# Optimization experiments

Measured on AMD Instinct MI355X. Metric: run time of the kernel, lower is better.

Reference implementation:

```python
import jax, jax.numpy as jnp
import numpy as np

N_NODES = 100000
N_EDGES = 1600000
D = 64
K = 10


def setup_inputs() -> dict:
    key = jax.random.key(0)
    k1, k2, k3, k4 = jax.random.split(key, 4)
    features = jax.random.normal(k1, (N_NODES, D), dtype=jnp.float32)
    s = jax.random.normal(k2, (D, 1), dtype=jnp.float32)
    src = jax.random.randint(k3, (N_EDGES,), 0, N_NODES, dtype=jnp.int64)
    dst = jax.random.randint(k4, (N_EDGES,), 0, N_NODES, dtype=jnp.int64)
    return {"features": features, "s": s, "src": src, "dst": dst, "k": K}


def reference(features, s, src, dst, k):
    n = features.shape[0]
    # symmetric degree norm: deg_in clamped at 1, norm = deg^{-1/2}
    deg = jax.ops.segment_sum(jnp.ones_like(dst, dtype=features.dtype), dst,
                              num_segments=n)
    norm = jnp.power(jnp.maximum(deg, 1.0), -0.5)[:, None]  # [N,1]

    def step(h, _):
        h = h * norm
        # copy_u + sum: scatter-add src features into dst nodes (SpMM)
        h = jax.ops.segment_sum(h[src], dst, num_segments=n)
        h = h * norm
        return h, h

    _, hops = jax.lax.scan(step, features, None, length=k)  # [k,N,D]
    H = jnp.concatenate([features[None], hops], axis=0)      # [k+1,N,D]
    H = jnp.transpose(H, (1, 0, 2))                           # [N,k+1,D]
    # attention pooling: S = sigmoid(H @ s), out = S^T H
    S = jax.nn.sigmoid(jnp.einsum('nkd,d->nk', H, s[:, 0]))  # [N,k+1]
    out = jnp.einsum('nk,nkd->nd', S, H)                      # [N,D]
    return out
```

## Files before the change

### kernel.cpp

```cpp
#include <hip/hip_runtime.h>
#include <hip/hip_fp16.h>
#include <math.h>

#define D 64
#define RB 1024
#define EB 2048
#define NRMAX 128
#define KHOPS 10


typedef union { uint4 u; __half2 h[4]; } U4H;
typedef float vfloat2 __attribute__((ext_vector_type(2)));

__device__ __forceinline__ void acc_fp8x8(uint2 q, float* a) {
    vfloat2 r0 = __builtin_amdgcn_cvt_pk_f32_fp8(q.x, false);
    vfloat2 r1 = __builtin_amdgcn_cvt_pk_f32_fp8(q.x, true);
    vfloat2 r2 = __builtin_amdgcn_cvt_pk_f32_fp8(q.y, false);
    vfloat2 r3 = __builtin_amdgcn_cvt_pk_f32_fp8(q.y, true);
    a[0] += r0.x; a[1] += r0.y; a[2] += r1.x; a[3] += r1.y;
    a[4] += r2.x; a[5] += r2.y; a[6] += r3.x; a[7] += r3.y;
}

__device__ __forceinline__ uint2 pack_fp8x8(const float* v) {
    uint2 q;
    q.x = __builtin_amdgcn_cvt_pk_fp8_f32(v[0], v[1], 0, false);
    q.x = __builtin_amdgcn_cvt_pk_fp8_f32(v[2], v[3], q.x, true);
    q.y = __builtin_amdgcn_cvt_pk_fp8_f32(v[4], v[5], 0, false);
    q.y = __builtin_amdgcn_cvt_pk_fp8_f32(v[6], v[7], q.y, true);
    return q;
}


__global__ void countA(const int* __restrict__ dst, int* __restrict__ countsA_T,
                       int E, int NR, int NBLK) {
    __shared__ int hist[NRMAX];
    int t = threadIdx.x;
    for (int i = t; i < NR; i += 256) hist[i] = 0;
    __syncthreads();
    int base = blockIdx.x * EB + t;
    #pragma unroll
    for (int j = 0; j < EB / 256; ++j) {
        int e = base + j * 256;
        if (e < E) atomicAdd(&hist[dst[e] >> 10], 1);
    }
    __syncthreads();
    for (int i = t; i < NR; i += 256) countsA_T[i * NBLK + blockIdx.x] = hist[i];
}

__global__ void block_sums(const int* __restrict__ arr, int* __restrict__ bsum, int n) {
    int base = blockIdx.x * 1024;
    int t = threadIdx.x;
    int v = 0;
    #pragma unroll
    for (int j = 0; j < 4; ++j) {
        int i = base + t + j * 256;
        if (i < n) v += arr[i];
    }
    #pragma unroll
    for (int m = 32; m >= 1; m >>= 1) v += __shfl_xor(v, m, 64);
    __shared__ int ws[4];
    if ((t & 63) == 0) ws[t >> 6] = v;
    __syncthreads();
    if (t == 0) bsum[blockIdx.x] = ws[0] + ws[1] + ws[2] + ws[3];
}

__global__ void scan_bsums(int* __restrict__ bsum, int nb) {
    __shared__ int tmp[1024];
    int t = threadIdx.x;
    int v = (t < nb) ? bsum[t] : 0;
    tmp[t] = v;
    __syncthreads();
    for (int off = 1; off < 1024; off <<= 1) {
        int x = (t >= off) ? tmp[t - off] : 0;
        __syncthreads();
        tmp[t] += x;
        __syncthreads();
    }
    if (t < nb) bsum[t] = tmp[t] - v;
}

__global__ void gen_scan2(const int* __restrict__ arr, const int* __restrict__ bsum,
                          int* __restrict__ out, int n) {
    __shared__ int tmp[1024];
    int base = blockIdx.x * 1024;
    int t = threadIdx.x;
    int i = base + t;
    int v = (i < n) ? arr[i] : 0;
    tmp[t] = v;
    __syncthreads();
    for (int off = 1; off < 1024; off <<= 1) {
        int x = (t >= off) ? tmp[t - off] : 0;
        __syncthreads();
        tmp[t] += x;
        __syncthreads();
    }
    if (i < n) out[i] = bsum[blockIdx.x] + tmp[t] - v;
}

__global__ void passA2(const int* __restrict__ src, const int* __restrict__ dst,
                       const int* __restrict__ baseA, unsigned int* __restrict__ ebuf2,
                       int E, int NR, int NBLK) {
    __shared__ int cur[NRMAX];
    int t = threadIdx.x;
    for (int i = t; i < NR; i += 256) cur[i] = baseA[i * NBLK + blockIdx.x];
    __syncthreads();
    int base = blockIdx.x * EB + t;
    #pragma unroll
    for (int j = 0; j < EB / 256; ++j) {
        int e = base + j * 256;
        if (e < E) {
            int v = dst[e];
            int pos = atomicAdd(&cur[v >> 10], 1);
            ebuf2[pos] = (unsigned int)src[e] | ((unsigned int)(v & (RB - 1)) << 17);
        }
    }
}

__global__ void range_build(const unsigned int* __restrict__ ebuf2,
                            const int* __restrict__ baseA,
                            int* __restrict__ offsets, float* __restrict__ norm,
                            int* __restrict__ csr, int N, int E, int NR, int NBLK) {
    __shared__ int cnt[RB];
    __shared__ int sc[RB];
    int rg = blockIdx.x;
    int t = threadIdx.x;
    int r0 = baseA[rg * NBLK];
    int r1 = (rg + 1 < NR) ? baseA[(rg + 1) * NBLK] : E;
    cnt[t] = 0;
    __syncthreads();
    for (int i = r0 + t; i < r1; i += RB)
        atomicAdd(&cnt[ebuf2[i] >> 17], 1);
    __syncthreads();
    int v = cnt[t];
    sc[t] = v;
    __syncthreads();
    for (int off = 1; off < RB; off <<= 1) {
        int x = (t >= off) ? sc[t - off] : 0;
        __syncthreads();
        sc[t] += x;
        __syncthreads();
    }
    int excl = sc[t] - v;
    int node = rg * RB + t;
    if (node < N) {
        offsets[node] = r0 + excl;
        norm[node] = rsqrtf((float)(v > 1 ? v : 1));
    }
    if (rg == NR - 1 && t == 0) offsets[N] = E;
    __syncthreads();
    cnt[t] = r0 + excl;
    __syncthreads();
    for (int i = r0 + t; i < r1; i += RB) {
        unsigned int u = ebuf2[i];
        int pos = atomicAdd(&cnt[u >> 17], 1);
        csr[pos] = (int)(u & 0x1FFFFu);
    }
}


__global__ void hop0(const float4* __restrict__ feat, const float* __restrict__ s,
                     const float* __restrict__ norm, uint4* __restrict__ g0,
                     uint2* __restrict__ p0, float4* __restrict__ out,
                     int n, int do_pool, int write8) {
    int t = blockIdx.x * blockDim.x + threadIdx.x;
    int node = t >> 3;
    int l = t & 7;
    if (node >= n) return;
    float4 f0 = feat[node * 16 + 2 * l];
    float4 f1 = feat[node * 16 + 2 * l + 1];
    float nv = norm[node];
    float v[8] = {f0.x * nv, f0.y * nv, f0.z * nv, f0.w * nv,
                  f1.x * nv, f1.y * nv, f1.z * nv, f1.w * nv};
    U4H P;
    P.h[0] = __floats2half2_rn(v[0], v[1]);
    P.h[1] = __floats2half2_rn(v[2], v[3]);
    P.h[2] = __floats2half2_rn(v[4], v[5]);
    P.h[3] = __floats2half2_rn(v[6], v[7]);
    g0[node * 8 + l] = P.u;
    if (write8) p0[node * 8 + l] = pack_fp8x8(v);
    if (do_pool) {
        const float4* s4 = (const float4*)s;
        float4 a = s4[2 * l], b = s4[2 * l + 1];
        float dot = f0.x * a.x + f0.y * a.y + f0.z * a.z + f0.w * a.w
                  + f1.x * b.x + f1.y * b.y + f1.z * b.z + f1.w * b.w;
        #pragma unroll
        for (int m = 1; m <= 4; m <<= 1) dot += __shfl_xor(dot, m, 64);
        float sig = 1.0f / (1.0f + expf(-dot));
        out[node * 16 + 2 * l]     = make_float4(sig * f0.x, sig * f0.y, sig * f0.z, sig * f0.w);
        out[node * 16 + 2 * l + 1] = make_float4(sig * f1.x, sig * f1.y, sig * f1.z, sig * f1.w);
    }
}


#define FP8_SLOT(K)                                                        \
    {                                                                      \
        int e0 = g + 8 * (K), e1 = e0 + 8;                                 \
        int u0 = __shfl(idx, e0, 64);                                      \
        int u1 = __shfl(idx, e1, 64);                                      \
        uint2 q0 = gin8[(size_t)u0 * 8 + l];                               \
        uint2 q1 = gin8[(size_t)u1 * 8 + l];                               \
        if (e0 < dcap) acc_fp8x8(q0, acc);                                 \
        if (e1 < dcap) acc_fp8x8(q1, acc);                                 \
    }

__global__ void spmm_hop_fp8(const uint2* __restrict__ gin8,
                             const int* __restrict__ offsets,
                             const int* __restrict__ csr,
                             const float* __restrict__ norm,
                             uint4* __restrict__ gout16,
                             uint2* __restrict__ gout8,
                             int n, int write8) {
    int lane = threadIdx.x & 63;
    int node = blockIdx.x * 4 + (threadIdx.x >> 6);
    if (node >= n) return;
    int g = lane >> 3;
    int l = lane & 7;
    int beg = offsets[node], end = offsets[node + 1];
    int deg = end - beg;
    int dcap = deg < 64 ? deg : 64;
    int idx = (lane < dcap) ? csr[beg + lane] : 0;

    float acc[8] = {0.f, 0.f, 0.f, 0.f, 0.f, 0.f, 0.f, 0.f};
    FP8_SLOT(0)
    if (dcap > 16) FP8_SLOT(2)
    if (dcap > 32) { FP8_SLOT(4) FP8_SLOT(6) }
    for (int i = beg + 64 + g; i < end; i += 8) {
        acc_fp8x8(gin8[(size_t)csr[i] * 8 + l], acc);
    }

    #pragma unroll
    for (int m = 8; m <= 32; m <<= 1) {
        #pragma unroll
        for (int jj = 0; jj < 8; ++jj) acc[jj] += __shfl_xor(acc[jj], m, 64);
    }

    if (g == 0) {
        float nv = norm[node];
        float gv[8];
        #pragma unroll
        for (int jj = 0; jj < 8; ++jj) gv[jj] = acc[jj] * nv * nv;
        U4H P;
        P.h[0] = __floats2half2_rn(gv[0], gv[1]);
        P.h[1] = __floats2half2_rn(gv[2], gv[3]);
        P.h[2] = __floats2half2_rn(gv[4], gv[5]);
        P.h[3] = __floats2half2_rn(gv[6], gv[7]);
        gout16[node * 8 + l] = P.u;
        if (write8) gout8[node * 8 + l] = pack_fp8x8(gv);
    }
}


__global__ void spmm_hop(const uint4* __restrict__ gin, const int* __restrict__ offsets,
                         const int* __restrict__ csr, const float* __restrict__ norm,
                         const float* __restrict__ s, uint4* __restrict__ gout,
                         float4* __restrict__ out, int n, int do_pool, int write_g) {
    int lane = threadIdx.x & 63;
    int node = blockIdx.x * 4 + (threadIdx.x >> 6);
    if (node >= n) return;
    int g = lane >> 3;
    int l = lane & 7;
    int beg = offsets[node], end = offsets[node + 1];
    int deg = end - beg;
    int dcap = deg < 64 ? deg : 64;
    int idx = (lane < dcap) ? csr[beg + lane] : 0;

    __half2 z = __floats2half2_rn(0.f, 0.f);
    __half2 ah0 = z, ah1 = z, ah2 = z, ah3 = z;
    {
        int e0 = g, e1 = g + 8, e2 = g + 16, e3 = g + 24;
        int u0 = __shfl(idx, e0, 64);
        int u1 = __shfl(idx, e1, 64);
        int u2 = __shfl(idx, e2, 64);
        int u3 = __shfl(idx, e3, 64);
        U4H A, B, C, Dd;
        A.u = gin[(size_t)u0 * 8 + l];
        B.u = gin[(size_t)u1 * 8 + l];
        C.u = gin[(size_t)u2 * 8 + l];
        Dd.u = gin[(size_t)u3 * 8 + l];
        if (e0 < dcap) { ah0 = __hadd2(ah0, A.h[0]); ah1 = __hadd2(ah1, A.h[1]); ah2 = __hadd2(ah2, A.h[2]); ah3 = __hadd2(ah3, A.h[3]); }
        if (e1 < dcap) { ah0 = __hadd2(ah0, B.h[0]); ah1 = __hadd2(ah1, B.h[1]); ah2 = __hadd2(ah2, B.h[2]); ah3 = __hadd2(ah3, B.h[3]); }
        if (e2 < dcap) { ah0 = __hadd2(ah0, C.h[0]); ah1 = __hadd2(ah1, C.h[1]); ah2 = __hadd2(ah2, C.h[2]); ah3 = __hadd2(ah3, C.h[3]); }
        if (e3 < dcap) { ah0 = __hadd2(ah0, Dd.h[0]); ah1 = __hadd2(ah1, Dd.h[1]); ah2 = __hadd2(ah2, Dd.h[2]); ah3 = __hadd2(ah3, Dd.h[3]); }
    }
    if (dcap > 32) {
        int e0 = g + 32, e1 = g + 40, e2 = g + 48, e3 = g + 56;
        int u0 = __shfl(idx, e0, 64);
        int u1 = __shfl(idx, e1, 64);
        int u2 = __shfl(idx, e2, 64);
        int u3 = __shfl(idx, e3, 64);
        U4H A, B, C, Dd;
        A.u = gin[(size_t)u0 * 8 + l];
        B.u = gin[(size_t)u1 * 8 + l];
        C.u = gin[(size_t)u2 * 8 + l];
        Dd.u = gin[(size_t)u3 * 8 + l];
        if (e0 < dcap) { ah0 = __hadd2(ah0, A.h[0]); ah1 = __hadd2(ah1, A.h[1]); ah2 = __hadd2(ah2, A.h[2]); ah3 = __hadd2(ah3, A.h[3]); }
        if (e1 < dcap) { ah0 = __hadd2(ah0, B.h[0]); ah1 = __hadd2(ah1, B.h[1]); ah2 = __hadd2(ah2, B.h[2]); ah3 = __hadd2(ah3, B.h[3]); }
        if (e2 < dcap) { ah0 = __hadd2(ah0, C.h[0]); ah1 = __hadd2(ah1, C.h[1]); ah2 = __hadd2(ah2, C.h[2]); ah3 = __hadd2(ah3, C.h[3]); }
        if (e3 < dcap) { ah0 = __hadd2(ah0, Dd.h[0]); ah1 = __hadd2(ah1, Dd.h[1]); ah2 = __hadd2(ah2, Dd.h[2]); ah3 = __hadd2(ah3, Dd.h[3]); }
    }

    float2 q0 = __half22float2(ah0), q1 = __half22float2(ah1);
    float2 q2 = __half22float2(ah2), q3 = __half22float2(ah3);
    float acc[8] = {q0.x, q0.y, q1.x, q1.y, q2.x, q2.y, q3.x, q3.y};

    for (int i = beg + 64 + g; i < end; i += 8) {
        U4H P; P.u = gin[(size_t)csr[i] * 8 + l];
        float2 a0 = __half22float2(P.h[0]), a1 = __half22float2(P.h[1]);
        float2 a2 = __half22float2(P.h[2]), a3 = __half22float2(P.h[3]);
        acc[0] += a0.x; acc[1] += a0.y; acc[2] += a1.x; acc[3] += a1.y;
        acc[4] += a2.x; acc[5] += a2.y; acc[6] += a3.x; acc[7] += a3.y;
    }

    #pragma unroll
    for (int m = 8; m <= 32; m <<= 1) {
        #pragma unroll
        for (int jj = 0; jj < 8; ++jj) acc[jj] += __shfl_xor(acc[jj], m, 64);
    }

    float nv = norm[node];
    float h[8];
    #pragma unroll
    for (int jj = 0; jj < 8; ++jj) h[jj] = acc[jj] * nv;

    float sig = 0.f;
    if (do_pool) {
        const float4* s4 = (const float4*)s;
        float4 a = s4[2 * l], b = s4[2 * l + 1];
        float dot = h[0] * a.x + h[1] * a.y + h[2] * a.z + h[3] * a.w
                  + h[4] * b.x + h[5] * b.y + h[6] * b.z + h[7] * b.w;
        #pragma unroll
        for (int m = 1; m <= 4; m <<= 1) dot += __shfl_xor(dot, m, 64);
        sig = 1.0f / (1.0f + expf(-dot));
    }

    if (g == 0) {
        if (write_g) {
            U4H P;
            P.h[0] = __floats2half2_rn(h[0] * nv, h[1] * nv);
            P.h[1] = __floats2half2_rn(h[2] * nv, h[3] * nv);
            P.h[2] = __floats2half2_rn(h[4] * nv, h[5] * nv);
            P.h[3] = __floats2half2_rn(h[6] * nv, h[7] * nv);
            gout[node * 8 + l] = P.u;
        }
        if (do_pool) {
            float4 o0 = out[node * 16 + 2 * l];
            float4 o1 = out[node * 16 + 2 * l + 1];
            o0.x += sig * h[0]; o0.y += sig * h[1]; o0.z += sig * h[2]; o0.w += sig * h[3];
            o1.x += sig * h[4]; o1.y += sig * h[5]; o1.z += sig * h[6]; o1.w += sig * h[7];
            out[node * 16 + 2 * l]     = o0;
            out[node * 16 + 2 * l + 1] = o1;
        }
    }
}


__global__ void pool_epilogue(const uint4* __restrict__ gbase, size_t gstride,
                              const float* __restrict__ norm,
                              const float* __restrict__ s,
                              float4* __restrict__ out, int N) {
    int t0 = blockIdx.x * blockDim.x + threadIdx.x;
    int node = t0 >> 3;
    int l = t0 & 7;
    if (node >= N) return;
    float inv_nv = 1.0f / norm[node];
    const float4* s4 = (const float4*)s;
    float4 sa = s4[2 * l], sb = s4[2 * l + 1];
    float o[8] = {0.f, 0.f, 0.f, 0.f, 0.f, 0.f, 0.f, 0.f};
    for (int t = 0; t <= KHOPS; ++t) {
        U4H P; P.u = gbase[(size_t)t * gstride + (size_t)node * 8 + l];
        float2 a0 = __half22float2(P.h[0]), a1 = __half22float2(P.h[1]);
        float2 a2 = __half22float2(P.h[2]), a3 = __half22float2(P.h[3]);
        float gf[8] = {a0.x, a0.y, a1.x, a1.y, a2.x, a2.y, a3.x, a3.y};
        float dot = gf[0] * sa.x + gf[1] * sa.y + gf[2] * sa.z + gf[3] * sa.w
                  + gf[4] * sb.x + gf[5] * sb.y + gf[6] * sb.z + gf[7] * sb.w;
        #pragma unroll
        for (int m = 1; m <= 4; m <<= 1) dot += __shfl_xor(dot, m, 64);
        float sig = 1.0f / (1.0f + expf(-dot * inv_nv));
        float sc = sig * inv_nv;
        #pragma unroll
        for (int j = 0; j < 8; ++j) o[j] += sc * gf[j];
    }
    out[node * 16 + 2 * l]     = make_float4(o[0], o[1], o[2], o[3]);
    out[node * 16 + 2 * l + 1] = make_float4(o[4], o[5], o[6], o[7]);
}


extern "C" void kernel_launch(void* const* d_in, const int* in_sizes, int n_in,
                              void* d_out, int out_size, void* d_ws, size_t ws_size,
                              hipStream_t stream) {
    const float* feat = (const float*)d_in[0];
    const float* s    = (const float*)d_in[1];
    const int*   src  = (const int*)d_in[2];
    const int*   dst  = (const int*)d_in[3];

    int N = in_sizes[0] / D;
    int E = in_sizes[2];
    int NR   = (N + RB - 1) / RB;
    int NBLK = (E + EB - 1) / EB;
    int M    = NR * NBLK;
    int nchA = (M + 1023) / 1024;

    int*   offsets  = (int*)d_ws;
    int*   csr      = offsets + (N + 1);
    float* norm     = (float*)(csr + E);
    int*   countsA  = (int*)(norm + N);
    int*   baseA    = countsA + M;
    int*   bsumA    = baseA + M;
    uintptr_t p = (uintptr_t)(bsumA + nchA);
    p = (p + 255) & ~(uintptr_t)255;
    uint4* gbase = (uint4*)p;
    size_t gstride = (size_t)N * 8;
    uint2* pbase = (uint2*)(gbase + (size_t)(KHOPS + 1) * gstride);
    size_t pstride = (size_t)N * 8;

    size_t fixed_bytes = (uintptr_t)gbase - (uintptr_t)d_ws;
    size_t need_f16 = (size_t)(KHOPS + 1) * gstride * sizeof(uint4);
    size_t need_fp8 = 2 * pstride * sizeof(uint2);
    int mode;
    if (ws_size >= fixed_bytes + need_f16 + need_fp8) mode = 2;
    else if (ws_size >= fixed_bytes + need_f16)       mode = 1;
    else                                              mode = 0;

    unsigned int* ebuf2 = (unsigned int*)(gbase + gstride);

    countA<<<NBLK, 256, 0, stream>>>(dst, countsA, E, NR, NBLK);
    block_sums<<<nchA, 256, 0, stream>>>(countsA, bsumA, M);
    scan_bsums<<<1, 1024, 0, stream>>>(bsumA, nchA);
    gen_scan2<<<nchA, 1024, 0, stream>>>(countsA, bsumA, baseA, M);
    passA2<<<NBLK, 256, 0, stream>>>(src, dst, baseA, ebuf2, E, NR, NBLK);
    range_build<<<NR, RB, 0, stream>>>(ebuf2, baseA, offsets, norm, csr, N, E, NR, NBLK);

    float4* outp = (float4*)d_out;
    int nb_node8 = (N * 8 + 255) / 256;
    int nb_spmm  = (N + 3) / 4;

    if (mode == 2) {
        hop0<<<nb_node8, 256, 0, stream>>>((const float4*)feat, s, norm, gbase,
                                           pbase, outp, N, 0, 1);
        for (int t = 0; t < KHOPS; ++t) {
            spmm_hop_fp8<<<nb_spmm, 256, 0, stream>>>(
                pbase + (size_t)(t & 1) * pstride, offsets, csr, norm,
                gbase + (size_t)(t + 1) * gstride,
                pbase + (size_t)((t + 1) & 1) * pstride,
                N, (t < KHOPS - 1) ? 1 : 0);
        }
        pool_epilogue<<<nb_node8, 256, 0, stream>>>(gbase, gstride, norm, s, outp, N);
    } else if (mode == 1) {
        hop0<<<nb_node8, 256, 0, stream>>>((const float4*)feat, s, norm, gbase,
                                           (uint2*)nullptr, outp, N, 0, 0);
        for (int t = 0; t < KHOPS; ++t) {
            spmm_hop<<<nb_spmm, 256, 0, stream>>>(
                gbase + (size_t)t * gstride, offsets, csr, norm, s,
                gbase + (size_t)(t + 1) * gstride, outp, N, 0, 1);
        }
        pool_epilogue<<<nb_node8, 256, 0, stream>>>(gbase, gstride, norm, s, outp, N);
    } else {
        hop0<<<nb_node8, 256, 0, stream>>>((const float4*)feat, s, norm, gbase,
                                           (uint2*)nullptr, outp, N, 1, 0);
        uint4* gin = gbase;
        uint4* gout = gbase + gstride;
        for (int t = 0; t < KHOPS; ++t) {
            spmm_hop<<<nb_spmm, 256, 0, stream>>>(
                gin, offsets, csr, norm, s, gout, outp, N, 1, (t < KHOPS - 1) ? 1 : 0);
            uint4* tmp = gin; gin = gout; gout = tmp;
        }
    }
}
```

Measured before the change: 546.0 us.

## Make fp8 SpMM hop persistent with grid-stride nodes and prefetched next indices

```diff
diff --git a/kernel.cpp b/kernel.cpp
--- a/kernel.cpp
+++ b/kernel.cpp
@@ -7,6 +7,7 @@
 #define EB 2048
 #define NRMAX 128
 #define KHOPS 10
+#define HOP_BLOCKS 2048
 
 
 typedef union { uint4 u; __half2 h[4]; } U4H;
@@ -192,164 +193,96 @@
 }
 
 
-#define FP8_SLOT(K)                                                        \
-    {                                                                      \
-        int e0 = g + 8 * (K), e1 = e0 + 8;                                 \
-        int u0 = __shfl(idx, e0, 64);                                      \
-        int u1 = __shfl(idx, e1, 64);                                      \
-        uint2 q0 = gin8[(size_t)u0 * 8 + l];                               \
-        uint2 q1 = gin8[(size_t)u1 * 8 + l];                               \
-        if (e0 < dcap) acc_fp8x8(q0, acc);                                 \
-        if (e1 < dcap) acc_fp8x8(q1, acc);                                 \
-    }
-
 __global__ void spmm_hop_fp8(const uint2* __restrict__ gin8,
                              const int* __restrict__ offsets,
                              const int* __restrict__ csr,
                              const float* __restrict__ norm,
                              uint4* __restrict__ gout16,
                              uint2* __restrict__ gout8,
-                             int n, int write8) {
+                             int n, int write8, int nwaves) {
     int lane = threadIdx.x & 63;
-    int node = blockIdx.x * 4 + (threadIdx.x >> 6);
-    if (node >= n) return;
+    int wave = (int)((blockIdx.x * blockDim.x + threadIdx.x) >> 6);
     int g = lane >> 3;
     int l = lane & 7;
-    int beg = offsets[node], end = offsets[node + 1];
-    int deg = end - beg;
-    int dcap = deg < 64 ? deg : 64;
-    int idx = (lane < dcap) ? csr[beg + lane] : 0;
-
-    float acc[8] = {0.f, 0.f, 0.f, 0.f, 0.f, 0.f, 0.f, 0.f};
-    FP8_SLOT(0)
-    if (dcap > 16) FP8_SLOT(2)
-    if (dcap > 32) { FP8_SLOT(4) FP8_SLOT(6) }
-    for (int i = beg + 64 + g; i < end; i += 8) {
-        acc_fp8x8(gin8[(size_t)csr[i] * 8 + l], acc);
-    }
-
-    #pragma unroll
-    for (int m = 8; m <= 32; m <<= 1) {
+
+    int node = wave;
+    if (node >= n) return;
+    int beg = offsets[node];
+    int end = offsets[node + 1];
+    int dcap0 = end - beg; if (dcap0 > 64) dcap0 = 64;
+    int idx = (lane < dcap0) ? csr[beg + lane] : 0;
+
+    while (true) {
+        int deg = end - beg;
+        int dcap = deg < 64 ? deg : 64;
+
+        int nnode = node + nwaves;
+        bool have_next = nnode < n;
+        int nbeg = 0, nend = 0;
+        if (have_next) { nbeg = offsets[nnode]; nend = offsets[nnode + 1]; }
+
+        float acc[8] = {0.f, 0.f, 0.f, 0.f, 0.f, 0.f, 0.f, 0.f};
+        {
+            int e0 = g, e1 = g + 8, e2 = g + 16, e3 = g + 24;
+            int u0 = __shfl(idx, e0, 64);
+            int u1 = __shfl(idx, e1, 64);
+            int u2 = __shfl(idx, e2, 64);
+            int u3 = __shfl(idx, e3, 64);
+            uint2 q0 = gin8[(size_t)u0 * 8 + l];
+            uint2 q1 = gin8[(size_t)u1 * 8 + l];
+            uint2 q2 = gin8[(size_t)u2 * 8 + l];
+            uint2 q3 = gin8[(size_t)u3 * 8 + l];
+            if (e0 < dcap) acc_fp8x8(q0, acc);
+            if (e1 < dcap) acc_fp8x8(q1, acc);
+            if (e2 < dcap) acc_fp8x8(q2, acc);
+            if (e3 < dcap) acc_fp8x8(q3, acc);
+        }
+        int nidx = 0;
+        if (have_next) {
+            int ncap = nend - nbeg; if (ncap > 64) ncap = 64;
+            nidx = (lane < ncap) ? csr[nbeg + lane] : 0;
+        }
+        if (dcap > 32) {
+            int e0 = g + 32, e1 = g + 40, e2 = g + 48, e3 = g + 56;
+            int u0 = __shfl(idx, e0, 64);
+            int u1 = __shfl(idx, e1, 64);
+            int u2 = __shfl(idx, e2, 64);
+            int u3 = __shfl(idx, e3, 64);
+            uint2 q0 = gin8[(size_t)u0 * 8 + l];
+            uint2 q1 = gin8[(size_t)u1 * 8 + l];
+            uint2 q2 = gin8[(size_t)u2 * 8 + l];
+            uint2 q3 = gin8[(size_t)u3 * 8 + l];
+            if (e0 < dcap) acc_fp8x8(q0, acc);
+            if (e1 < dcap) acc_fp8x8(q1, acc);
+            if (e2 < dcap) acc_fp8x8(q2, acc);
+            if (e3 < dcap) acc_fp8x8(q3, acc);
+        }
+        for (int i = beg + 64 + g; i < end; i += 8) {
+            acc_fp8x8(gin8[(size_t)csr[i] * 8 + l], acc);
+        }
+
         #pragma unroll
-        for (int jj = 0; jj < 8; ++jj) acc[jj] += __shfl_xor(acc[jj], m, 64);
-    }
-
-    if (g == 0) {
-        float nv = norm[node];
-        float gv[8];
-        #pragma unroll
-        for (int jj = 0; jj < 8; ++jj) gv[jj] = acc[jj] * nv * nv;
-        U4H P;
-        P.h[0] = __floats2half2_rn(gv[0], gv[1]);
-        P.h[1] = __floats2half2_rn(gv[2], gv[3]);
-        P.h[2] = __floats2half2_rn(gv[4], gv[5]);
-        P.h[3] = __floats2half2_rn(gv[6], gv[7]);
-        gout16[node * 8 + l] = P.u;
-        if (write8) gout8[node * 8 + l] = pack_fp8x8(gv);
-    }
-}
-
-
-__global__ void spmm_hop(const uint4* __restrict__ gin, const int* __restrict__ offsets,
-                         const int* __restrict__ csr, const float* __restrict__ norm,
-                         const float* __restrict__ s, uint4* __restrict__ gout,
-                         float4* __restrict__ out, int n, int do_pool, int write_g) {
-    int lane = threadIdx.x & 63;
-    int node = blockIdx.x * 4 + (threadIdx.x >> 6);
-    if (node >= n) return;
-    int g = lane >> 3;
-    int l = lane & 7;
-    int beg = offsets[node], end = offsets[node + 1];
-    int deg = end - beg;
-    int dcap = deg < 64 ? deg : 64;
-    int idx = (lane < dcap) ? csr[beg + lane] : 0;
-
-    __half2 z = __floats2half2_rn(0.f, 0.f);
-    __half2 ah0 = z, ah1 = z, ah2 = z, ah3 = z;
-    {
-        int e0 = g, e1 = g + 8, e2 = g + 16, e3 = g + 24;
-        int u0 = __shfl(idx, e0, 64);
-        int u1 = __shfl(idx, e1, 64);
-        int u2 = __shfl(idx, e2, 64);
-        int u3 = __shfl(idx, e3, 64);
-        U4H A, B, C, Dd;
-        A.u = gin[(size_t)u0 * 8 + l];
-        B.u = gin[(size_t)u1 * 8 + l];
-        C.u = gin[(size_t)u2 * 8 + l];
-        Dd.u = gin[(size_t)u3 * 8 + l];
-        if (e0 < dcap) { ah0 = __hadd2(ah0, A.h[0]); ah1 = __hadd2(ah1, A.h[1]); ah2 = __hadd2(ah2, A.h[2]); ah3 = __hadd2(ah3, A.h[3]); }
-        if (e1 < dcap) { ah0 = __hadd2(ah0, B.h[0]); ah1 = __hadd2(ah1, B.h[1]); ah2 = __hadd2(ah2, B.h[2]); ah3 = __hadd2(ah3, B.h[3]); }
-        if (e2 < dcap) { ah0 = __hadd2(ah0, C.h[0]); ah1 = __hadd2(ah1, C.h[1]); ah2 = __hadd2(ah2, C.h[2]); ah3 = __hadd2(ah3, C.h[3]); }
-        if (e3 < dcap) { ah0 = __hadd2(ah0, Dd.h[0]); ah1 = __hadd2(ah1, Dd.h[1]); ah2 = __hadd2(ah2, Dd.h[2]); ah3 = __hadd2(ah3, Dd.h[3]); }
-    }
-    if (dcap > 32) {
-        int e0 = g + 32, e1 = g + 40, e2 = g + 48, e3 = g + 56;
-        int u0 = __shfl(idx, e0, 64);
-        int u1 = __shfl(idx, e1, 64);
-        int u2 = __shfl(idx, e2, 64);
-        int u3 = __shfl(idx, e3, 64);
-        U4H A, B, C, Dd;
-        A.u = gin[(size_t)u0 * 8 + l];
-        B.u = gin[(size_t)u1 * 8 + l];
-        C.u = gin[(size_t)u2 * 8 + l];
-        Dd.u = gin[(size_t)u3 * 8 + l];
-        if (e0 < dcap) { ah0 = __hadd2(ah0, A.h[0]); ah1 = __hadd2(ah1, A.h[1]); ah2 = __hadd2(ah2, A.h[2]); ah3 = __hadd2(ah3, A.h[3]); }
-        if (e1 < dcap) { ah0 = __hadd2(ah0, B.h[0]); ah1 = __hadd2(ah1, B.h[1]); ah2 = __hadd2(ah2, B.h[2]); ah3 = __hadd2(ah3, B.h[3]); }
-        if (e2 < dcap) { ah0 = __hadd2(ah0, C.h[0]); ah1 = __hadd2(ah1, C.h[1]); ah2 = __hadd2(ah2, C.h[2]); ah3 = __hadd2(ah3, C.h[3]); }
-        if (e3 < dcap) { ah0 = __hadd2(ah0, Dd.h[0]); ah1 = __hadd2(ah1, Dd.h[1]); ah2 = __hadd2(ah2, Dd.h[2]); ah3 = __hadd2(ah3, Dd.h[3]); }
-    }
-
-    float2 q0 = __half22float2(ah0), q1 = __half22float2(ah1);
-    float2 q2 = __half22float2(ah2), q3 = __half22float2(ah3);
-    float acc[8] = {q0.x, q0.y, q1.x, q1.y, q2.x, q2.y, q3.x, q3.y};
-
-    for (int i = beg + 64 + g; i < end; i += 8) {
-        U4H P; P.u = gin[(size_t)csr[i] * 8 + l];
-        float2 a0 = __half22float2(P.h[0]), a1 = __half22float2(P.h[1]);
-        float2 a2 = __half22float2(P.h[2]), a3 = __half22float2(P.h[3]);
-        acc[0] += a0.x; acc[1] += a0.y; acc[2] += a1.x; acc[3] += a1.y;
-        acc[4] += a2.x; acc[5] += a2.y; acc[6] += a3.x; acc[7] += a3.y;
-    }
-
-    #pragma unroll
-    for (int m = 8; m <= 32; m <<= 1) {
-        #pragma unroll
-        for (int jj = 0; jj < 8; ++jj) acc[jj] += __shfl_xor(acc[jj], m, 64);
-    }
-
-    float nv = norm[node];
-    float h[8];
-    #pragma unroll
-    for (int jj = 0; jj < 8; ++jj) h[jj] = acc[jj] * nv;
-
-    float sig = 0.f;
-    if (do_pool) {
-        const float4* s4 = (const float4*)s;
-        float4 a = s4[2 * l], b = s4[2 * l + 1];
-        float dot = h[0] * a.x + h[1] * a.y + h[2] * a.z + h[3] * a.w
-                  + h[4] * b.x + h[5] * b.y + h[6] * b.z + h[7] * b.w;
-        #pragma unroll
-        for (int m = 1; m <= 4; m <<= 1) dot += __shfl_xor(dot, m, 64);
-        sig = 1.0f / (1.0f + expf(-dot));
-    }
-
-    if (g == 0) {
-        if (write_g) {
+        for (int m = 8; m <= 32; m <<= 1) {
+            #pragma unroll
+            for (int jj = 0; jj < 8; ++jj) acc[jj] += __shfl_xor(acc[jj], m, 64);
+        }
+
+        if (g == 0) {
+            float nv = norm[node];
+            float gv[8];
+            #pragma unroll
+            for (int jj = 0; jj < 8; ++jj) gv[jj] = acc[jj] * nv * nv;
             U4H P;
-            P.h[0] = __floats2half2_rn(h[0] * nv, h[1] * nv);
-            P.h[1] = __floats2half2_rn(h[2] * nv, h[3] * nv);
-            P.h[2] = __floats2half2_rn(h[4] * nv, h[5] * nv);
-            P.h[3] = __floats2half2_rn(h[6] * nv, h[7] * nv);
-            gout[node * 8 + l] = P.u;
-        }
-        if (do_pool) {
-            float4 o0 = out[node * 16 + 2 * l];
-            float4 o1 = out[node * 16 + 2 * l + 1];
-            o0.x += sig * h[0]; o0.y += sig * h[1]; o0.z += sig * h[2]; o0.w += sig * h[3];
-            o1.x += sig * h[4]; o1.y += sig * h[5]; o1.z += sig * h[6]; o1.w += sig * h[7];
-            out[node * 16 + 2 * l]     = o0;
-            out[node * 16 + 2 * l + 1] = o1;
-        }
+            P.h[0] = __floats2half2_rn(gv[0], gv[1]);
+            P.h[1] = __floats2half2_rn(gv[2], gv[3]);
+            P.h[2] = __floats2half2_rn(gv[4], gv[5]);
+            P.h[3] = __floats2half2_rn(gv[6], gv[7]);
+            gout16[node * 8 + l] = P.u;
+            if (write8) gout8[node * 8 + l] = pack_fp8x8(gv);
+        }
+
+        if (!have_next) break;
+        node = nnode; beg = nbeg; end = nend; idx = nidx;
     }
 }
 
@@ -385,6 +318,110 @@
 }
 
 
+__global__ void spmm_hop(const uint4* __restrict__ gin, const int* __restrict__ offsets,
+                         const int* __restrict__ csr, const float* __restrict__ norm,
+                         const float* __restrict__ s, uint4* __restrict__ gout,
+                         float4* __restrict__ out, int n, int do_pool, int write_g) {
+    int lane = threadIdx.x & 63;
+    int node = blockIdx.x * 4 + (threadIdx.x >> 6);
+    if (node >= n) return;
+    int g = lane >> 3;
+    int l = lane & 7;
+    int beg = offsets[node], end = offsets[node + 1];
+    int deg = end - beg;
+    int dcap = deg < 64 ? deg : 64;
+    int idx = (lane < dcap) ? csr[beg + lane] : 0;
+
+    __half2 z = __floats2half2_rn(0.f, 0.f);
+    __half2 ah0 = z, ah1 = z, ah2 = z, ah3 = z;
+    {
+        int e0 = g, e1 = g + 8, e2 = g + 16, e3 = g + 24;
+        int u0 = __shfl(idx, e0, 64);
+        int u1 = __shfl(idx, e1, 64);
+        int u2 = __shfl(idx, e2, 64);
+        int u3 = __shfl(idx, e3, 64);
+        U4H A, B, C, Dd;
+        A.u = gin[(size_t)u0 * 8 + l];
+        B.u = gin[(size_t)u1 * 8 + l];
+        C.u = gin[(size_t)u2 * 8 + l];
+        Dd.u = gin[(size_t)u3 * 8 + l];
+        if (e0 < dcap) { ah0 = __hadd2(ah0, A.h[0]); ah1 = __hadd2(ah1, A.h[1]); ah2 = __hadd2(ah2, A.h[2]); ah3 = __hadd2(ah3, A.h[3]); }
+        if (e1 < dcap) { ah0 = __hadd2(ah0, B.h[0]); ah1 = __hadd2(ah1, B.h[1]); ah2 = __hadd2(ah2, B.h[2]); ah3 = __hadd2(ah3, B.h[3]); }
+        if (e2 < dcap) { ah0 = __hadd2(ah0, C.h[0]); ah1 = __hadd2(ah1, C.h[1]); ah2 = __hadd2(ah2, C.h[2]); ah3 = __hadd2(ah3, C.h[3]); }
+        if (e3 < dcap) { ah0 = __hadd2(ah0, Dd.h[0]); ah1 = __hadd2(ah1, Dd.h[1]); ah2 = __hadd2(ah2, Dd.h[2]); ah3 = __hadd2(ah3, Dd.h[3]); }
+    }
+    if (dcap > 32) {
+        int e0 = g + 32, e1 = g + 40, e2 = g + 48, e3 = g + 56;
+        int u0 = __shfl(idx, e0, 64);
+        int u1 = __shfl(idx, e1, 64);
+        int u2 = __shfl(idx, e2, 64);
+        int u3 = __shfl(idx, e3, 64);
+        U4H A, B, C, Dd;
+        A.u = gin[(size_t)u0 * 8 + l];
+        B.u = gin[(size_t)u1 * 8 + l];
+        C.u = gin[(size_t)u2 * 8 + l];
+        Dd.u = gin[(size_t)u3 * 8 + l];
+        if (e0 < dcap) { ah0 = __hadd2(ah0, A.h[0]); ah1 = __hadd2(ah1, A.h[1]); ah2 = __hadd2(ah2, A.h[2]); ah3 = __hadd2(ah3, A.h[3]); }
+        if (e1 < dcap) { ah0 = __hadd2(ah0, B.h[0]); ah1 = __hadd2(ah1, B.h[1]); ah2 = __hadd2(ah2, B.h[2]); ah3 = __hadd2(ah3, B.h[3]); }
+        if (e2 < dcap) { ah0 = __hadd2(ah0, C.h[0]); ah1 = __hadd2(ah1, C.h[1]); ah2 = __hadd2(ah2, C.h[2]); ah3 = __hadd2(ah3, C.h[3]); }
+        if (e3 < dcap) { ah0 = __hadd2(ah0, Dd.h[0]); ah1 = __hadd2(ah1, Dd.h[1]); ah2 = __hadd2(ah2, Dd.h[2]); ah3 = __hadd2(ah3, Dd.h[3]); }
+    }
+
+    float2 q0 = __half22float2(ah0), q1 = __half22float2(ah1);
+    float2 q2 = __half22float2(ah2), q3 = __half22float2(ah3);
+    float acc[8] = {q0.x, q0.y, q1.x, q1.y, q2.x, q2.y, q3.x, q3.y};
+
+    for (int i = beg + 64 + g; i < end; i += 8) {
+        U4H P; P.u = gin[(size_t)csr[i] * 8 + l];
+        float2 a0 = __half22float2(P.h[0]), a1 = __half22float2(P.h[1]);
+        float2 a2 = __half22float2(P.h[2]), a3 = __half22float2(P.h[3]);
+        acc[0] += a0.x; acc[1] += a0.y; acc[2] += a1.x; acc[3] += a1.y;
+        acc[4] += a2.x; acc[5] += a2.y; acc[6] += a3.x; acc[7] += a3.y;
+    }
+
+    #pragma unroll
+    for (int m = 8; m <= 32; m <<= 1) {
+        #pragma unroll
+        for (int jj = 0; jj < 8; ++jj) acc[jj] += __shfl_xor(acc[jj], m, 64);
+    }
+
+    float nv = norm[node];
+    float h[8];
+    #pragma unroll
+    for (int jj = 0; jj < 8; ++jj) h[jj] = acc[jj] * nv;
+
+    float sig = 0.f;
+    if (do_pool) {
+        const float4* s4 = (const float4*)s;
+        float4 a = s4[2 * l], b = s4[2 * l + 1];
+        float dot = h[0] * a.x + h[1] * a.y + h[2] * a.z + h[3] * a.w
+                  + h[4] * b.x + h[5] * b.y + h[6] * b.z + h[7] * b.w;
+        #pragma unroll
+        for (int m = 1; m <= 4; m <<= 1) dot += __shfl_xor(dot, m, 64);
+        sig = 1.0f / (1.0f + expf(-dot));
+    }
+
+    if (g == 0) {
+        if (write_g) {
+            U4H P;
+            P.h[0] = __floats2half2_rn(h[0] * nv, h[1] * nv);
+            P.h[1] = __floats2half2_rn(h[2] * nv, h[3] * nv);
+            P.h[2] = __floats2half2_rn(h[4] * nv, h[5] * nv);
+            P.h[3] = __floats2half2_rn(h[6] * nv, h[7] * nv);
+            gout[node * 8 + l] = P.u;
+        }
+        if (do_pool) {
+            float4 o0 = out[node * 16 + 2 * l];
+            float4 o1 = out[node * 16 + 2 * l + 1];
+            o0.x += sig * h[0]; o0.y += sig * h[1]; o0.z += sig * h[2]; o0.w += sig * h[3];
+            o1.x += sig * h[4]; o1.y += sig * h[5]; o1.z += sig * h[6]; o1.w += sig * h[7];
+            out[node * 16 + 2 * l]     = o0;
+            out[node * 16 + 2 * l + 1] = o1;
+        }
+    }
+}
+
+
 extern "C" void kernel_launch(void* const* d_in, const int* in_sizes, int n_in,
                               void* d_out, int out_size, void* d_ws, size_t ws_size,
                               hipStream_t stream) {
@@ -433,16 +470,17 @@
     float4* outp = (float4*)d_out;
     int nb_node8 = (N * 8 + 255) / 256;
     int nb_spmm  = (N + 3) / 4;
+    int nwaves   = HOP_BLOCKS * 4;
 
     if (mode == 2) {
         hop0<<<nb_node8, 256, 0, stream>>>((const float4*)feat, s, norm, gbase,
                                            pbase, outp, N, 0, 1);
         for (int t = 0; t < KHOPS; ++t) {
-            spmm_hop_fp8<<<nb_spmm, 256, 0, stream>>>(
+            spmm_hop_fp8<<<HOP_BLOCKS, 256, 0, stream>>>(
                 pbase + (size_t)(t & 1) * pstride, offsets, csr, norm,
                 gbase + (size_t)(t + 1) * gstride,
                 pbase + (size_t)((t + 1) & 1) * pstride,
-                N, (t < KHOPS - 1) ? 1 : 0);
+                N, (t < KHOPS - 1) ? 1 : 0, nwaves);
         }
         pool_epilogue<<<nb_node8, 256, 0, stream>>>(gbase, gstride, norm, s, outp, N);
     } else if (mode == 1) {
```

Result: slower. 557.0 us (+2.0%).

## Split FP8 SpMM gather into two source-index phases and add nontemporal hints

Applied to the files above, without the earlier changes.

```diff
diff --git a/kernel.cpp b/kernel.cpp
--- a/kernel.cpp
+++ b/kernel.cpp
@@ -11,6 +11,7 @@
 
 typedef union { uint4 u; __half2 h[4]; } U4H;
 typedef float vfloat2 __attribute__((ext_vector_type(2)));
+typedef unsigned int uiv4 __attribute__((ext_vector_type(4)));
 
 __device__ __forceinline__ void acc_fp8x8(uint2 q, float* a) {
     vfloat2 r0 = __builtin_amdgcn_cvt_pk_f32_fp8(q.x, false);
@@ -192,24 +193,13 @@
 }
 
 
-#define FP8_SLOT(K)                                                        \
-    {                                                                      \
-        int e0 = g + 8 * (K), e1 = e0 + 8;                                 \
-        int u0 = __shfl(idx, e0, 64);                                      \
-        int u1 = __shfl(idx, e1, 64);                                      \
-        uint2 q0 = gin8[(size_t)u0 * 8 + l];                               \
-        uint2 q1 = gin8[(size_t)u1 * 8 + l];                               \
-        if (e0 < dcap) acc_fp8x8(q0, acc);                                 \
-        if (e1 < dcap) acc_fp8x8(q1, acc);                                 \
-    }
-
 __global__ void spmm_hop_fp8(const uint2* __restrict__ gin8,
                              const int* __restrict__ offsets,
                              const int* __restrict__ csr,
                              const float* __restrict__ norm,
                              uint4* __restrict__ gout16,
                              uint2* __restrict__ gout8,
-                             int n, int write8) {
+                             int n, int write8, int half) {
     int lane = threadIdx.x & 63;
     int node = blockIdx.x * 4 + (threadIdx.x >> 6);
     if (node >= n) return;
@@ -218,12 +208,60 @@
     int beg = offsets[node], end = offsets[node + 1];
     int deg = end - beg;
     int dcap = deg < 64 ? deg : 64;
-    int idx = (lane < dcap) ? csr[beg + lane] : 0;
+    int idx = (lane < dcap) ? __builtin_nontemporal_load(&csr[beg + lane]) : 0;
 
     float acc[8] = {0.f, 0.f, 0.f, 0.f, 0.f, 0.f, 0.f, 0.f};
-    FP8_SLOT(0)
-    if (dcap > 16) FP8_SLOT(2)
-    if (dcap > 32) { FP8_SLOT(4) FP8_SLOT(6) }
+    #pragma unroll
+    for (int ph = 0; ph < 2; ++ph) {
+        int lo = ph ? half : 0;
+        int hi = ph ? n : half;
+        {
+            int e0 = g, e1 = g + 8, e2 = g + 16, e3 = g + 24;
+            int u0 = __shfl(idx, e0, 64);
+            int u1 = __shfl(idx, e1, 64);
+            int u2 = __shfl(idx, e2, 64);
+            int u3 = __shfl(idx, e3, 64);
+            bool i0 = (e0 < dcap) && (u0 >= lo) && (u0 < hi);
+            bool i1 = (e1 < dcap) && (u1 >= lo) && (u1 < hi);
+            bool i2 = (e2 < dcap) && (u2 >= lo) && (u2 < hi);
+            bool i3 = (e3 < dcap) && (u3 >= lo) && (u3 < hi);
+            int a0 = i0 ? u0 : lo;
+            int a1 = i1 ? u1 : lo;
+            int a2 = i2 ? u2 : lo;
+            int a3 = i3 ? u3 : lo;
+            uint2 q0 = gin8[(size_t)a0 * 8 + l];
+            uint2 q1 = gin8[(size_t)a1 * 8 + l];
+            uint2 q2 = gin8[(size_t)a2 * 8 + l];
+            uint2 q3 = gin8[(size_t)a3 * 8 + l];
+            if (i0) acc_fp8x8(q0, acc);
+            if (i1) acc_fp8x8(q1, acc);
+            if (i2) acc_fp8x8(q2, acc);
+            if (i3) acc_fp8x8(q3, acc);
+        }
+        if (dcap > 32) {
+            int e0 = g + 32, e1 = g + 40, e2 = g + 48, e3 = g + 56;
+            int u0 = __shfl(idx, e0, 64);
+            int u1 = __shfl(idx, e1, 64);
+            int u2 = __shfl(idx, e2, 64);
+            int u3 = __shfl(idx, e3, 64);
+            bool i0 = (e0 < dcap) && (u0 >= lo) && (u0 < hi);
+            bool i1 = (e1 < dcap) && (u1 >= lo) && (u1 < hi);
+            bool i2 = (e2 < dcap) && (u2 >= lo) && (u2 < hi);
+            bool i3 = (e3 < dcap) && (u3 >= lo) && (u3 < hi);
+            int a0 = i0 ? u0 : lo;
+            int a1 = i1 ? u1 : lo;
+            int a2 = i2 ? u2 : lo;
+            int a3 = i3 ? u3 : lo;
+            uint2 q0 = gin8[(size_t)a0 * 8 + l];
+            uint2 q1 = gin8[(size_t)a1 * 8 + l];
+            uint2 q2 = gin8[(size_t)a2 * 8 + l];
+            uint2 q3 = gin8[(size_t)a3 * 8 + l];
+            if (i0) acc_fp8x8(q0, acc);
+            if (i1) acc_fp8x8(q1, acc);
+            if (i2) acc_fp8x8(q2, acc);
+            if (i3) acc_fp8x8(q3, acc);
+        }
+    }
     for (int i = beg + 64 + g; i < end; i += 8) {
         acc_fp8x8(gin8[(size_t)csr[i] * 8 + l], acc);
     }
@@ -244,112 +282,8 @@
         P.h[1] = __floats2half2_rn(gv[2], gv[3]);
         P.h[2] = __floats2half2_rn(gv[4], gv[5]);
         P.h[3] = __floats2half2_rn(gv[6], gv[7]);
-        gout16[node * 8 + l] = P.u;
+        __builtin_nontemporal_store(*(const uiv4*)&P.u, (uiv4*)&gout16[node * 8 + l]);
         if (write8) gout8[node * 8 + l] = pack_fp8x8(gv);
-    }
-}
-
-
-__global__ void spmm_hop(const uint4* __restrict__ gin, const int* __restrict__ offsets,
-                         const int* __restrict__ csr, const float* __restrict__ norm,
-                         const float* __restrict__ s, uint4* __restrict__ gout,
-                         float4* __restrict__ out, int n, int do_pool, int write_g) {
-    int lane = threadIdx.x & 63;
-    int node = blockIdx.x * 4 + (threadIdx.x >> 6);
-    if (node >= n) return;
-    int g = lane >> 3;
-    int l = lane & 7;
-    int beg = offsets[node], end = offsets[node + 1];
-    int deg = end - beg;
-    int dcap = deg < 64 ? deg : 64;
-    int idx = (lane < dcap) ? csr[beg + lane] : 0;
-
-    __half2 z = __floats2half2_rn(0.f, 0.f);
-    __half2 ah0 = z, ah1 = z, ah2 = z, ah3 = z;
-    {
-        int e0 = g, e1 = g + 8, e2 = g + 16, e3 = g + 24;
-        int u0 = __shfl(idx, e0, 64);
-        int u1 = __shfl(idx, e1, 64);
-        int u2 = __shfl(idx, e2, 64);
-        int u3 = __shfl(idx, e3, 64);
-        U4H A, B, C, Dd;
-        A.u = gin[(size_t)u0 * 8 + l];
-        B.u = gin[(size_t)u1 * 8 + l];
-        C.u = gin[(size_t)u2 * 8 + l];
-        Dd.u = gin[(size_t)u3 * 8 + l];
-        if (e0 < dcap) { ah0 = __hadd2(ah0, A.h[0]); ah1 = __hadd2(ah1, A.h[1]); ah2 = __hadd2(ah2, A.h[2]); ah3 = __hadd2(ah3, A.h[3]); }
-        if (e1 < dcap) { ah0 = __hadd2(ah0, B.h[0]); ah1 = __hadd2(ah1, B.h[1]); ah2 = __hadd2(ah2, B.h[2]); ah3 = __hadd2(ah3, B.h[3]); }
-        if (e2 < dcap) { ah0 = __hadd2(ah0, C.h[0]); ah1 = __hadd2(ah1, C.h[1]); ah2 = __hadd2(ah2, C.h[2]); ah3 = __hadd2(ah3, C.h[3]); }
-        if (e3 < dcap) { ah0 = __hadd2(ah0, Dd.h[0]); ah1 = __hadd2(ah1, Dd.h[1]); ah2 = __hadd2(ah2, Dd.h[2]); ah3 = __hadd2(ah3, Dd.h[3]); }
-    }
-    if (dcap > 32) {
-        int e0 = g + 32, e1 = g + 40, e2 = g + 48, e3 = g + 56;
-        int u0 = __shfl(idx, e0, 64);
-        int u1 = __shfl(idx, e1, 64);
-        int u2 = __shfl(idx, e2, 64);
-        int u3 = __shfl(idx, e3, 64);
-        U4H A, B, C, Dd;
-        A.u = gin[(size_t)u0 * 8 + l];
-        B.u = gin[(size_t)u1 * 8 + l];
-        C.u = gin[(size_t)u2 * 8 + l];
-        Dd.u = gin[(size_t)u3 * 8 + l];
-        if (e0 < dcap) { ah0 = __hadd2(ah0, A.h[0]); ah1 = __hadd2(ah1, A.h[1]); ah2 = __hadd2(ah2, A.h[2]); ah3 = __hadd2(ah3, A.h[3]); }
-        if (e1 < dcap) { ah0 = __hadd2(ah0, B.h[0]); ah1 = __hadd2(ah1, B.h[1]); ah2 = __hadd2(ah2, B.h[2]); ah3 = __hadd2(ah3, B.h[3]); }
-        if (e2 < dcap) { ah0 = __hadd2(ah0, C.h[0]); ah1 = __hadd2(ah1, C.h[1]); ah2 = __hadd2(ah2, C.h[2]); ah3 = __hadd2(ah3, C.h[3]); }
-        if (e3 < dcap) { ah0 = __hadd2(ah0, Dd.h[0]); ah1 = __hadd2(ah1, Dd.h[1]); ah2 = __hadd2(ah2, Dd.h[2]); ah3 = __hadd2(ah3, Dd.h[3]); }
-    }
-
-    float2 q0 = __half22float2(ah0), q1 = __half22float2(ah1);
-    float2 q2 = __half22float2(ah2), q3 = __half22float2(ah3);
-    float acc[8] = {q0.x, q0.y, q1.x, q1.y, q2.x, q2.y, q3.x, q3.y};
-
-    for (int i = beg + 64 + g; i < end; i += 8) {
-        U4H P; P.u = gin[(size_t)csr[i] * 8 + l];
-        float2 a0 = __half22float2(P.h[0]), a1 = __half22float2(P.h[1]);
-        float2 a2 = __half22float2(P.h[2]), a3 = __half22float2(P.h[3]);
-        acc[0] += a0.x; acc[1] += a0.y; acc[2] += a1.x; acc[3] += a1.y;
-        acc[4] += a2.x; acc[5] += a2.y; acc[6] += a3.x; acc[7] += a3.y;
-    }
-
-    #pragma unroll
-    for (int m = 8; m <= 32; m <<= 1) {
-        #pragma unroll
-        for (int jj = 0; jj < 8; ++jj) acc[jj] += __shfl_xor(acc[jj], m, 64);
-    }
-
-    float nv = norm[node];
-    float h[8];
-    #pragma unroll
-    for (int jj = 0; jj < 8; ++jj) h[jj] = acc[jj] * nv;
-
-    float sig = 0.f;
-    if (do_pool) {
-        const float4* s4 = (const float4*)s;
-        float4 a = s4[2 * l], b = s4[2 * l + 1];
-        float dot = h[0] * a.x + h[1] * a.y + h[2] * a.z + h[3] * a.w
-                  + h[4] * b.x + h[5] * b.y + h[6] * b.z + h[7] * b.w;
-        #pragma unroll
-        for (int m = 1; m <= 4; m <<= 1) dot += __shfl_xor(dot, m, 64);
-        sig = 1.0f / (1.0f + expf(-dot));
-    }
-
-    if (g == 0) {
-        if (write_g) {
-            U4H P;
-            P.h[0] = __floats2half2_rn(h[0] * nv, h[1] * nv);
-            P.h[1] = __floats2half2_rn(h[2] * nv, h[3] * nv);
-            P.h[2] = __floats2half2_rn(h[4] * nv, h[5] * nv);
-            P.h[3] = __floats2half2_rn(h[6] * nv, h[7] * nv);
-            gout[node * 8 + l] = P.u;
-        }
-        if (do_pool) {
-            float4 o0 = out[node * 16 + 2 * l];
-            float4 o1 = out[node * 16 + 2 * l + 1];
-            o0.x += sig * h[0]; o0.y += sig * h[1]; o0.z += sig * h[2]; o0.w += sig * h[3];
-            o1.x += sig * h[4]; o1.y += sig * h[5]; o1.z += sig * h[6]; o1.w += sig * h[7];
-            out[node * 16 + 2 * l]     = o0;
-            out[node * 16 + 2 * l + 1] = o1;
-        }
     }
 }
 
@@ -385,6 +319,110 @@
 }
 
 
+__global__ void spmm_hop(const uint4* __restrict__ gin, const int* __restrict__ offsets,
+                         const int* __restrict__ csr, const float* __restrict__ norm,
+                         const float* __restrict__ s, uint4* __restrict__ gout,
+                         float4* __restrict__ out, int n, int do_pool, int write_g) {
+    int lane = threadIdx.x & 63;
+    int node = blockIdx.x * 4 + (threadIdx.x >> 6);
+    if (node >= n) return;
+    int g = lane >> 3;
+    int l = lane & 7;
+    int beg = offsets[node], end = offsets[node + 1];
+    int deg = end - beg;
+    int dcap = deg < 64 ? deg : 64;
+    int idx = (lane < dcap) ? csr[beg + lane] : 0;
+
+    __half2 z = __floats2half2_rn(0.f, 0.f);
+    __half2 ah0 = z, ah1 = z, ah2 = z, ah3 = z;
+    {
+        int e0 = g, e1 = g + 8, e2 = g + 16, e3 = g + 24;
+        int u0 = __shfl(idx, e0, 64);
+        int u1 = __shfl(idx, e1, 64);
+        int u2 = __shfl(idx, e2, 64);
+        int u3 = __shfl(idx, e3, 64);
+        U4H A, B, C, Dd;
+        A.u = gin[(size_t)u0 * 8 + l];
+        B.u = gin[(size_t)u1 * 8 + l];
+        C.u = gin[(size_t)u2 * 8 + l];
+        Dd.u = gin[(size_t)u3 * 8 + l];
+        if (e0 < dcap) { ah0 = __hadd2(ah0, A.h[0]); ah1 = __hadd2(ah1, A.h[1]); ah2 = __hadd2(ah2, A.h[2]); ah3 = __hadd2(ah3, A.h[3]); }
+        if (e1 < dcap) { ah0 = __hadd2(ah0, B.h[0]); ah1 = __hadd2(ah1, B.h[1]); ah2 = __hadd2(ah2, B.h[2]); ah3 = __hadd2(ah3, B.h[3]); }
+        if (e2 < dcap) { ah0 = __hadd2(ah0, C.h[0]); ah1 = __hadd2(ah1, C.h[1]); ah2 = __hadd2(ah2, C.h[2]); ah3 = __hadd2(ah3, C.h[3]); }
+        if (e3 < dcap) { ah0 = __hadd2(ah0, Dd.h[0]); ah1 = __hadd2(ah1, Dd.h[1]); ah2 = __hadd2(ah2, Dd.h[2]); ah3 = __hadd2(ah3, Dd.h[3]); }
+    }
+    if (dcap > 32) {
+        int e0 = g + 32, e1 = g + 40, e2 = g + 48, e3 = g + 56;
+        int u0 = __shfl(idx, e0, 64);
+        int u1 = __shfl(idx, e1, 64);
+        int u2 = __shfl(idx, e2, 64);
+        int u3 = __shfl(idx, e3, 64);
+        U4H A, B, C, Dd;
+        A.u = gin[(size_t)u0 * 8 + l];
+        B.u = gin[(size_t)u1 * 8 + l];
+        C.u = gin[(size_t)u2 * 8 + l];
+        Dd.u = gin[(size_t)u3 * 8 + l];
+        if (e0 < dcap) { ah0 = __hadd2(ah0, A.h[0]); ah1 = __hadd2(ah1, A.h[1]); ah2 = __hadd2(ah2, A.h[2]); ah3 = __hadd2(ah3, A.h[3]); }
+        if (e1 < dcap) { ah0 = __hadd2(ah0, B.h[0]); ah1 = __hadd2(ah1, B.h[1]); ah2 = __hadd2(ah2, B.h[2]); ah3 = __hadd2(ah3, B.h[3]); }
+        if (e2 < dcap) { ah0 = __hadd2(ah0, C.h[0]); ah1 = __hadd2(ah1, C.h[1]); ah2 = __hadd2(ah2, C.h[2]); ah3 = __hadd2(ah3, C.h[3]); }
+        if (e3 < dcap) { ah0 = __hadd2(ah0, Dd.h[0]); ah1 = __hadd2(ah1, Dd.h[1]); ah2 = __hadd2(ah2, Dd.h[2]); ah3 = __hadd2(ah3, Dd.h[3]); }
+    }
+
+    float2 q0 = __half22float2(ah0), q1 = __half22float2(ah1);
+    float2 q2 = __half22float2(ah2), q3 = __half22float2(ah3);
+    float acc[8] = {q0.x, q0.y, q1.x, q1.y, q2.x, q2.y, q3.x, q3.y};
+
+    for (int i = beg + 64 + g; i < end; i += 8) {
+        U4H P; P.u = gin[(size_t)csr[i] * 8 + l];
+        float2 a0 = __half22float2(P.h[0]), a1 = __half22float2(P.h[1]);
+        float2 a2 = __half22float2(P.h[2]), a3 = __half22float2(P.h[3]);
+        acc[0] += a0.x; acc[1] += a0.y; acc[2] += a1.x; acc[3] += a1.y;
+        acc[4] += a2.x; acc[5] += a2.y; acc[6] += a3.x; acc[7] += a3.y;
+    }
+
+    #pragma unroll
+    for (int m = 8; m <= 32; m <<= 1) {
+        #pragma unroll
+        for (int jj = 0; jj < 8; ++jj) acc[jj] += __shfl_xor(acc[jj], m, 64);
+    }
+
+    float nv = norm[node];
+    float h[8];
+    #pragma unroll
+    for (int jj = 0; jj < 8; ++jj) h[jj] = acc[jj] * nv;
+
+    float sig = 0.f;
+    if (do_pool) {
+        const float4* s4 = (const float4*)s;
+        float4 a = s4[2 * l], b = s4[2 * l + 1];
+        float dot = h[0] * a.x + h[1] * a.y + h[2] * a.z + h[3] * a.w
+                  + h[4] * b.x + h[5] * b.y + h[6] * b.z + h[7] * b.w;
+        #pragma unroll
+        for (int m = 1; m <= 4; m <<= 1) dot += __shfl_xor(dot, m, 64);
+        sig = 1.0f / (1.0f + expf(-dot));
+    }
+
+    if (g == 0) {
+        if (write_g) {
+            U4H P;
+            P.h[0] = __floats2half2_rn(h[0] * nv, h[1] * nv);
+            P.h[1] = __floats2half2_rn(h[2] * nv, h[3] * nv);
+            P.h[2] = __floats2half2_rn(h[4] * nv, h[5] * nv);
+            P.h[3] = __floats2half2_rn(h[6] * nv, h[7] * nv);
+            gout[node * 8 + l] = P.u;
+        }
+        if (do_pool) {
+            float4 o0 = out[node * 16 + 2 * l];
+            float4 o1 = out[node * 16 + 2 * l + 1];
+            o0.x += sig * h[0]; o0.y += sig * h[1]; o0.z += sig * h[2]; o0.w += sig * h[3];
+            o1.x += sig * h[4]; o1.y += sig * h[5]; o1.z += sig * h[6]; o1.w += sig * h[7];
+            out[node * 16 + 2 * l]     = o0;
+            out[node * 16 + 2 * l + 1] = o1;
+        }
+    }
+}
+
+
 extern "C" void kernel_launch(void* const* d_in, const int* in_sizes, int n_in,
                               void* d_out, int out_size, void* d_ws, size_t ws_size,
                               hipStream_t stream) {
@@ -433,6 +471,7 @@
     float4* outp = (float4*)d_out;
     int nb_node8 = (N * 8 + 255) / 256;
     int nb_spmm  = (N + 3) / 4;
+    int half     = (N + 1) / 2;
 
     if (mode == 2) {
         hop0<<<nb_node8, 256, 0, stream>>>((const float4*)feat, s, norm, gbase,
@@ -442,7 +481,7 @@
                 pbase + (size_t)(t & 1) * pstride, offsets, csr, norm,
                 gbase + (size_t)(t + 1) * gstride,
                 pbase + (size_t)((t + 1) & 1) * pstride,
-                N, (t < KHOPS - 1) ? 1 : 0);
+                N, (t < KHOPS - 1) ? 1 : 0, half);
         }
         pool_epilogue<<<nb_node8, 256, 0, stream>>>(gbase, gstride, norm, s, outp, N);
     } else if (mode == 1) {
```

Result: slower. 675.0 us (+23.6%).
